# Performance work log

Hardware: AMD Instinct MI355X
Metric: run time of the kernel (lower is better)

## Reference

```python
import jax, jax.numpy as jnp
import numpy as np

H = 8        # num_heads
KNN = 16     # k nearest neighbors
D = 256      # input_dim
LN_EPS = 1e-5


def _make_params(key, D):
    ks = jax.random.split(key, 10)
    def lin(k, din, dout):
        k1, k2 = jax.random.split(k)
        lim = 1.0 / np.sqrt(din)
        W = jax.random.uniform(k1, (din, dout), jnp.float32, -lim, lim)
        b = jax.random.uniform(k2, (dout,), jnp.float32, -lim, lim)
        return W, b
    Wq, bq = lin(ks[0], D, D)
    Wk, bk = lin(ks[1], D, D)
    Wv, bv = lin(ks[2], D, D)
    Wo1, bo1 = lin(ks[3], D, D)
    ln_g = jnp.ones((D,), jnp.float32)
    ln_b = jnp.zeros((D,), jnp.float32)
    Wo2, bo2 = lin(ks[4], D, D)
    return dict(Wq=Wq, bq=bq, Wk=Wk, bk=bk, Wv=Wv, bv=bv,
                Wo1=Wo1, bo1=bo1, ln_g=ln_g, ln_b=ln_b, Wo2=Wo2, bo2=bo2)


def setup_inputs() -> dict:
    key = jax.random.key(0)
    k1, k2, k3, k4, k5 = jax.random.split(key, 5)
    B, N, M = 2, 2048, 4096
    inp = {
        "src": jax.random.normal(k1, (B, N, 3), jnp.float32),
        "tgt": jax.random.normal(k2, (B, M, 3), jnp.float32),
        "src_fea": jax.random.normal(k3, (B, N, D), jnp.float32),
        "tgt_fea": jax.random.normal(k4, (B, M, D), jnp.float32),
    }
    inp.update(_make_params(k5, D))
    return inp


def _cdist(x, y):
    # Euclidean distance [B,N,M], matching torch.cdist(p=2)
    x2 = jnp.sum(x * x, axis=-1, keepdims=True)          # [B,N,1]
    y2 = jnp.sum(y * y, axis=-1, keepdims=True)          # [B,M,1]
    sq = x2 + jnp.swapaxes(y2, -1, -2) - 2.0 * jnp.einsum('bnc,bmc->bnm', x, y)
    return jnp.sqrt(jnp.maximum(sq, 0.0))


def _layernorm(x, g, b):
    mu = jnp.mean(x, axis=-1, keepdims=True)
    var = jnp.mean((x - mu) ** 2, axis=-1, keepdims=True)
    return (x - mu) * jax.lax.rsqrt(var + LN_EPS) * g + b


def reference(src, tgt, src_fea, tgt_fea, Wq, bq, Wk, bk, Wv, bv,
              Wo1, bo1, ln_g, ln_b, Wo2, bo2):
    B, N, Dm = src_fea.shape
    M = tgt.shape[1]
    dk = Dm // H
    scale = dk ** (-0.5)

    # kNN mask: distances [B,N,M], topk smallest -> boolean mask
    dist = _cdist(src, tgt)
    _, knn_idx = jax.lax.top_k(-dist, KNN)               # [B,N,KNN]
    bi = jnp.arange(B)[:, None, None]
    ni = jnp.arange(N)[None, :, None]
    mask = jnp.zeros((B, N, M), bool).at[bi, ni, knn_idx].set(True)

    # projections -> [B,H,*,dk]
    Q = (src_fea @ Wq + bq).reshape(B, N, H, dk).transpose(0, 2, 1, 3)
    K = (tgt_fea @ Wk + bk).reshape(B, M, H, dk).transpose(0, 2, 1, 3)
    V = (tgt_fea @ Wv + bv).reshape(B, M, H, dk).transpose(0, 2, 1, 3)

    scores = jnp.einsum('bhnd,bhmd->bhnm', Q, K) * scale
    scores = jnp.where(mask[:, None], scores, -jnp.inf)
    attn = jax.nn.softmax(scores, axis=-1)               # [B,H,N,M]

    out = jnp.einsum('bhnm,bhmd->bhnd', attn, V)
    out = out.transpose(0, 2, 1, 3).reshape(B, N, Dm)

    x = out + src_fea
    h = jax.nn.relu(_layernorm(x @ Wo1 + bo1, ln_g, ln_b))
    updated = h @ Wo2 + bo2

    avg_attn = jnp.mean(attn, axis=1)                    # [B,N,M]
    return updated, avg_attn
```

## Files before the change

kernel.cpp:

```cpp
#include <hip/hip_runtime.h>
#include <math.h>

#define BB 2
#define NN 2048
#define MM 4096
#define DD 256
#define HH 8
#define DK 32
#define KNN 16

typedef __attribute__((ext_vector_type(8))) short short8;
typedef __attribute__((ext_vector_type(4))) short short4v;
typedef __attribute__((ext_vector_type(4))) float f32x4;
typedef unsigned long long u64;
typedef unsigned short u16;

static __device__ __forceinline__ u16 f2bf(float f) {
    union { float f; unsigned u; } v; v.f = f;
    unsigned r = v.u + 0x7FFF + ((v.u >> 16) & 1);
    return (u16)(r >> 16);
}
static __device__ __forceinline__ float bf2f(u16 u) {
    union { unsigned u; float f; } v; v.u = ((unsigned)u) << 16;
    return v.f;
}

__global__ __launch_bounds__(256)
void prep(const float* W0, const float* W1, const float* W2, const float* W3, const float* W4,
          u16* O0, u16* O1, u16* O2, u16* O3, u16* O4,
          const float* __restrict__ tgt, float4* __restrict__ tgt4)
{
    __shared__ float tile[64][65];
    const int bid = blockIdx.x;
    const int t = threadIdx.x;
    if (bid >= 80) {
        const int i = (bid - 80) * 256 + t;
        const float x = tgt[i * 3 + 0], y = tgt[i * 3 + 1], z = tgt[i * 3 + 2];
        float4 o; o.x = x; o.y = y; o.z = z; o.w = x * x + y * y + z * z;
        tgt4[i] = o;
        return;
    }
    const int m = bid >> 4, tl = bid & 15;
    const int tr = (tl >> 2) * 64, tc = (tl & 3) * 64;
    const float* W = m == 0 ? W0 : m == 1 ? W1 : m == 2 ? W2 : m == 3 ? W3 : W4;
    u16*        O = m == 0 ? O0 : m == 1 ? O1 : m == 2 ? O2 : m == 3 ? O3 : O4;
    const int c = t & 63, r4 = t >> 6;
    #pragma unroll
    for (int i = 0; i < 16; ++i) {
        const int r = (r4 << 4) + i;
        tile[r][c] = W[(size_t)(tr + r) * 256 + tc + c];
    }
    __syncthreads();
    #pragma unroll
    for (int i = 0; i < 16; ++i) {
        const int cc = (r4 << 4) + i;
        O[(size_t)(tc + cc) * 256 + tr + c] = f2bf(tile[c][cc]);
    }
}

static __device__ __forceinline__ void gemm64_body(
    const float* __restrict__ A, size_t row0, const u16* __restrict__ WT, int col0,
    u16* As, u16* Bs, int t, f32x4 acc[2][2])
{
    const int lane = t & 63, w = t >> 6;
    const int wr = (w >> 1) * 32, wc = (w & 1) * 32;
    for (int k0 = 0; k0 < 256; k0 += 64) {
        #pragma unroll
        for (int e = 0; e < 2; ++e) {
            const int flat = t + (e << 8);
            const int r = flat >> 3, kc = (flat & 7) << 3;
            const int off = ((r << 7) + (kc << 1)) ^ ((r & 7) << 4);
            const float* ap = A + (row0 + r) * 256 + k0 + kc;
            float4 a0 = *(const float4*)ap;
            float4 a1 = *(const float4*)(ap + 4);
            short8 s;
            s[0] = (short)f2bf(a0.x); s[1] = (short)f2bf(a0.y);
            s[2] = (short)f2bf(a0.z); s[3] = (short)f2bf(a0.w);
            s[4] = (short)f2bf(a1.x); s[5] = (short)f2bf(a1.y);
            s[6] = (short)f2bf(a1.z); s[7] = (short)f2bf(a1.w);
            *(short8*)((char*)As + off) = s;
            *(short8*)((char*)Bs + off) = *(const short8*)(WT + (size_t)(col0 + r) * 256 + k0 + kc);
        }
        __syncthreads();
        #pragma unroll
        for (int kk = 0; kk < 64; kk += 32) {
            const int kbo = (kk + ((lane >> 4) << 3)) << 1;
            short8 af[2], bfr[2];
            #pragma unroll
            for (int i = 0; i < 2; ++i) {
                const int ra = wr + (i << 4) + (lane & 15);
                af[i]  = *(const short8*)((const char*)As + (((ra << 7) + kbo) ^ ((ra & 7) << 4)));
                const int rb = wc + (i << 4) + (lane & 15);
                bfr[i] = *(const short8*)((const char*)Bs + (((rb << 7) + kbo) ^ ((rb & 7) << 4)));
            }
            #pragma unroll
            for (int mi = 0; mi < 2; ++mi)
                #pragma unroll
                for (int ni = 0; ni < 2; ++ni)
                    acc[mi][ni] = __builtin_amdgcn_mfma_f32_16x16x32_bf16(af[mi], bfr[ni], acc[mi][ni], 0, 0, 0);
        }
        __syncthreads();
    }
}

__global__ __launch_bounds__(256, 4)
void mega_kernel(const float* __restrict__ src, const float* __restrict__ tgt,
                 const float4* __restrict__ tgt4,
                 int* __restrict__ knn_idx,
                 const float* __restrict__ tgt_fea, const float* __restrict__ src_fea,
                 const u16* __restrict__ WTq, const u16* __restrict__ WTkv,
                 const float* __restrict__ bq, const float* __restrict__ bk,
                 const float* __restrict__ bv,
                 float* __restrict__ Qb, u16* __restrict__ Kbf, u16* __restrict__ Vbf,
                 float* __restrict__ avg)
{
    __shared__ u16 As[64 * 64];
    __shared__ u16 Bs[64 * 64];
    const int bid = blockIdx.x;
    const int t = threadIdx.x;
    const int lane = t & 63;
    const int lid = bid / 11;
    const int role = bid % 11;

    if (role < 4) {
        const int kb = lid * 4 + role;
        const int bn = (kb << 2) + (t >> 6);
        const int b = bn >> 11;
        const float* sp = src + (size_t)bn * 3;
        const float px = sp[0], py = sp[1], pz = sp[2];
        const float x2 = px * px + py * py + pz * pz;
        const float4* t4 = tgt4 + (size_t)b * MM;
        unsigned key[64];
        unsigned s0 = 0xFFFFFFFFu, s1 = 0xFFFFFFFFu;
        #pragma unroll
        for (int j = 0; j < 64; ++j) {
            const int m = (j << 6) + lane;
            const float4 tp = t4[m];
            const float dot = px * tp.x + py * tp.y + pz * tp.z;
            float d = (x2 + tp.w) - 2.0f * dot;
            d = d > 0.f ? d : 0.f;
            const unsigned k = ((unsigned)fminf(d * 32768.0f, 1048574.0f) << 12) | (unsigned)m;
            key[j] = k;
            const unsigned hi = k > s0 ? k : s0;
            s0 = k < s0 ? k : s0;
            s1 = hi < s1 ? hi : s1;
        }
        unsigned lastPop = 0, mykey = 0;
        for (int sel = 0; sel < 20; ++sel) {
            if (s0 == 0xFFFFFFFFu) {
                unsigned bst = 0xFFFFFFFFu;
                #pragma unroll
                for (int j = 0; j < 64; ++j) {
                    const unsigned k = key[j];
                    bst = (k > lastPop && k < bst) ? k : bst;
                }
                s0 = bst;
            }
            unsigned best = s0;
            #pragma unroll
            for (int s2 = 32; s2; s2 >>= 1) {
                const unsigned o = __shfl_xor(best, s2, 64);
                best = o < best ? o : best;
            }
            if (lane == sel) mykey = best;
            if (s0 == best) {
                lastPop = s0;
                s0 = s1;
                s1 = 0xFFFFFFFFu;
            }
        }
        const int midx = (int)(mykey & 0xFFFu);
        const float* tb = tgt + (size_t)b * MM * 3;
        u64 ex = ~0ULL;
        if (lane < 20) {
            const float* tp = tb + (size_t)midx * 3;
            const double pxd = px, pyd = py, pzd = pz;
            const double tx = tp[0], ty = tp[1], tz = tp[2];
            const double x2d = pxd * pxd + pyd * pyd + pzd * pzd;
            const double y2d = tx * tx + ty * ty + tz * tz;
            const double dtd = pxd * tx + pyd * ty + pzd * tz;
            double dd = (x2d + y2d) - 2.0 * dtd;
            dd = dd > 0.0 ? dd : 0.0;
            ex = (((u64)__double_as_longlong(dd)) & ~0xFFFULL) | (u64)midx;
        }
        int rank = 0;
        #pragma unroll
        for (int i = 0; i < 20; ++i) {
            const u64 o = __shfl(ex, i, 64);
            rank += (o < ex) ? 1 : 0;
        }
        if (lane < 20 && rank < 16)
            knn_idx[(size_t)bn * KNN + rank] = midx;
        return;
    }

    if (role < 8) {
        const int kvb = lid * 4 + (role - 4);
        const size_t row0 = (size_t)(kvb >> 3) * 64;
        const int col0 = (kvb & 7) * 64;
        f32x4 acc[2][2] = {};
        gemm64_body(tgt_fea, row0, WTkv, col0, As, Bs, t, acc);
        const int w = t >> 6;
        const int wr = (w >> 1) * 32, wc = (w & 1) * 32;
        const bool isv = col0 >= 256;
        u16* ob = isv ? Vbf : Kbf;
        const float* bs = isv ? bv : bk;
        const int cb = (isv ? col0 - 256 : col0) + wc;
        const int cq = lane & 15, rq = (lane >> 4) << 2;
        #pragma unroll
        for (int ni = 0; ni < 2; ++ni) {
            const int c = cb + (ni << 4) + cq;
            const float bval = bs[c];
            #pragma unroll
            for (int mi = 0; mi < 2; ++mi) {
                const size_t r = row0 + wr + (mi << 4) + rq;
                #pragma unroll
                for (int e = 0; e < 4; ++e)
                    ob[(r + e) * 256 + c] = f2bf(acc[mi][ni][e] + bval);
            }
        }
        return;
    }

    if (role == 8) {
        const int qb = lid;
        const size_t row0 = (size_t)(qb >> 2) * 64;
        const int col0 = (qb & 3) * 64;
        f32x4 acc[2][2] = {};
        gemm64_body(src_fea, row0, WTq, col0, As, Bs, t, acc);
        const int w = t >> 6;
        const int wr = (w >> 1) * 32, wc = (w & 1) * 32;
        const int cq = lane & 15, rq = (lane >> 4) << 2;
        #pragma unroll
        for (int ni = 0; ni < 2; ++ni) {
            const int c = col0 + wc + (ni << 4) + cq;
            const float bval = bq[c];
            #pragma unroll
            for (int mi = 0; mi < 2; ++mi) {
                const size_t rbase = (row0 + wr + (mi << 4) + rq) * 256 + c;
                #pragma unroll
                for (int e = 0; e < 4; ++e)
                    Qb[rbase + (size_t)e * 256] = acc[mi][ni][e] + bval;
            }
        }
        return;
    }

    {
        const int zb = lid * 2 + (role - 9);
        f32x4 z = {0.f, 0.f, 0.f, 0.f};
        f32x4* pz = (f32x4*)avg;
        const int base = zb * 256 + t;
        #pragma unroll
        for (int i = 0; i < 32; ++i)
            pz[base + i * 131072] = z;
    }
}

__global__ __launch_bounds__(256)
void tail_kernel(const float* __restrict__ Q, const u16* __restrict__ Kb,
                 const u16* __restrict__ Vb, const int* __restrict__ knn_idx,
                 const float* __restrict__ src_fea,
                 const u16* __restrict__ WTo1, const float* __restrict__ bo1,
                 const float* __restrict__ lng, const float* __restrict__ lnb,
                 const u16* __restrict__ WTo2, const float* __restrict__ bo2,
                 float* __restrict__ updated, float* __restrict__ avg_attn)
{
    __shared__ float q_sh[4][256];
    __shared__ float pw_sh[4][8][17];
    __shared__ int   idx_sh[4][16];
    __shared__ u16   Xs[16 * 256];
    __shared__ u16   Hs[16 * 256];
    __shared__ float2 red2[4][4];
    const int t = threadIdx.x;
    const int w = t >> 6, lane = t & 63;
    const int r0 = blockIdx.x << 2;
    const int bn = r0 + w;
    const int b = bn >> 11;
    const int h = lane >> 3, k2 = lane & 7;

    {
        unsigned* xz = (unsigned*)Xs;
        unsigned* hz = (unsigned*)Hs;
        #pragma unroll
        for (int i = 0; i < 6; ++i) {
            xz[512 + t + i * 256] = 0u;
            hz[512 + t + i * 256] = 0u;
        }
    }

    *(float4*)&q_sh[w][lane << 2] = *(const float4*)(Q + (size_t)bn * 256 + (lane << 2));
    const int ia = knn_idx[(size_t)bn * KNN + k2];
    const int ib = knn_idx[(size_t)bn * KNN + 8 + k2];

    const u16* Ka = Kb + ((size_t)b * MM + ia) * 256 + h * DK;
    const u16* Kc = Kb + ((size_t)b * MM + ib) * 256 + h * DK;
    const float* qh = &q_sh[w][h * DK];
    float s0 = 0.f, s1 = 0.f;
    #pragma unroll
    for (int j = 0; j < DK; j += 8) {
        const short8 ka = *(const short8*)(Ka + j);
        const short8 kc = *(const short8*)(Kc + j);
        #pragma unroll
        for (int e = 0; e < 8; ++e) {
            const float qv = qh[j + e];
            s0 = fmaf(qv, bf2f((u16)ka[e]), s0);
            s1 = fmaf(qv, bf2f((u16)kc[e]), s1);
        }
    }
    s0 *= 0.17677669529663688f;
    s1 *= 0.17677669529663688f;

    float mx = fmaxf(s0, s1);
    mx = fmaxf(mx, __shfl_xor(mx, 1, 64));
    mx = fmaxf(mx, __shfl_xor(mx, 2, 64));
    mx = fmaxf(mx, __shfl_xor(mx, 4, 64));
    const float e0 = expf(s0 - mx), e1 = expf(s1 - mx);
    float sum = e0 + e1;
    sum += __shfl_xor(sum, 1, 64);
    sum += __shfl_xor(sum, 2, 64);
    sum += __shfl_xor(sum, 4, 64);
    const float inv = 1.0f / sum;
    const float p0 = e0 * inv, p1 = e1 * inv;

    float a0 = p0, a1 = p1;
    a0 += __shfl_xor(a0, 8, 64);  a1 += __shfl_xor(a1, 8, 64);
    a0 += __shfl_xor(a0, 16, 64); a1 += __shfl_xor(a1, 16, 64);
    a0 += __shfl_xor(a0, 32, 64); a1 += __shfl_xor(a1, 32, 64);
    if (h == 0) {
        avg_attn[(size_t)bn * MM + ia] = a0 * 0.125f;
        avg_attn[(size_t)bn * MM + ib] = a1 * 0.125f;
        idx_sh[w][k2] = ia;
        idx_sh[w][8 + k2] = ib;
    }
    pw_sh[w][h][k2] = p0;
    pw_sh[w][h][8 + k2] = p1;

    {
        const int d0 = lane << 2;
        const int h2 = lane >> 3;
        float o0 = 0.f, o1 = 0.f, o2 = 0.f, o3 = 0.f;
        #pragma unroll
        for (int k = 0; k < KNN; ++k) {
            const float p = pw_sh[w][h2][k];
            const int ik = idx_sh[w][k];
            const short4v v4 = *(const short4v*)(Vb + ((size_t)b * MM + ik) * 256 + d0);
            o0 = fmaf(p, bf2f((u16)v4[0]), o0);
            o1 = fmaf(p, bf2f((u16)v4[1]), o1);
            o2 = fmaf(p, bf2f((u16)v4[2]), o2);
            o3 = fmaf(p, bf2f((u16)v4[3]), o3);
        }
        const float4 sf = *(const float4*)(src_fea + (size_t)bn * 256 + d0);
        short4v xo;
        xo[0] = (short)f2bf(o0 + sf.x);
        xo[1] = (short)f2bf(o1 + sf.y);
        xo[2] = (short)f2bf(o2 + sf.z);
        xo[3] = (short)f2bf(o3 + sf.w);
        const int off = ((w << 9) + (d0 << 1)) ^ ((w & 7) << 4);
        *(short4v*)((char*)Xs + off) = xo;
    }
    __syncthreads();

    const int cq = lane & 15, ks = lane >> 4;
    f32x4 acc1[4] = {};
    #pragma unroll
    for (int s = 0; s < 4; ++s) {
        const int colB = (w << 6) + (s << 4) + cq;
        const u16* bp = WTo1 + (size_t)colB * 256;
        #pragma unroll
        for (int kk = 0; kk < 256; kk += 32) {
            const int k8 = kk + (ks << 3);
            const short8 af = *(const short8*)((const char*)Xs + (((cq << 9) + (k8 << 1)) ^ ((cq & 7) << 4)));
            const short8 bfrg = *(const short8*)(bp + k8);
            acc1[s] = __builtin_amdgcn_mfma_f32_16x16x32_bf16(af, bfrg, acc1[s], 0, 0, 0);
        }
        const float bval = bo1[colB];
        #pragma unroll
        for (int e = 0; e < 4; ++e) acc1[s][e] += bval;
    }
    {
        #pragma unroll
        for (int e = 0; e < 4; ++e) {
            float v = acc1[0][e] + acc1[1][e] + acc1[2][e] + acc1[3][e];
            float vv = acc1[0][e]*acc1[0][e] + acc1[1][e]*acc1[1][e]
                     + acc1[2][e]*acc1[2][e] + acc1[3][e]*acc1[3][e];
            v += __shfl_xor(v, 1, 64); vv += __shfl_xor(vv, 1, 64);
            v += __shfl_xor(v, 2, 64); vv += __shfl_xor(vv, 2, 64);
            v += __shfl_xor(v, 4, 64); vv += __shfl_xor(vv, 4, 64);
            v += __shfl_xor(v, 8, 64); vv += __shfl_xor(vv, 8, 64);
            if (ks == 0 && cq == 0) {
                float2 pr; pr.x = v; pr.y = vv;
                red2[w][e] = pr;
            }
        }
    }
    __syncthreads();
    if (ks == 0) {
        float g4[4], b4[4];
        #pragma unroll
        for (int s = 0; s < 4; ++s) {
            const int colB = (w << 6) + (s << 4) + cq;
            g4[s] = lng[colB]; b4[s] = lnb[colB];
        }
        #pragma unroll
        for (int e = 0; e < 4; ++e) {
            float S1 = 0.f, S2 = 0.f;
            #pragma unroll
            for (int w2 = 0; w2 < 4; ++w2) {
                const float2 pr = red2[w2][e];
                S1 += pr.x; S2 += pr.y;
            }
            const float mean = S1 * (1.0f / 256.0f);
            const float var = S2 * (1.0f / 256.0f) - mean * mean;
            const float rstd = 1.0f / sqrtf(var + 1e-5f);
            #pragma unroll
            for (int s = 0; s < 4; ++s) {
                const int colB = (w << 6) + (s << 4) + cq;
                const float y = (acc1[s][e] - mean) * rstd * g4[s] + b4[s];
                const int off = ((e << 9) + (colB << 1)) ^ ((e & 7) << 4);
                *(u16*)((char*)Hs + off) = f2bf(fmaxf(y, 0.0f));
            }
        }
    }
    __syncthreads();

    #pragma unroll
    for (int s = 0; s < 4; ++s) {
        const int colB = (w << 6) + (s << 4) + cq;
        const u16* bp = WTo2 + (size_t)colB * 256;
        f32x4 acc2 = {};
        #pragma unroll
        for (int kk = 0; kk < 256; kk += 32) {
            const int k8 = kk + (ks << 3);
            const short8 af = *(const short8*)((const char*)Hs + (((cq << 9) + (k8 << 1)) ^ ((cq & 7) << 4)));
            const short8 bfrg = *(const short8*)(bp + k8);
            acc2 = __builtin_amdgcn_mfma_f32_16x16x32_bf16(af, bfrg, acc2, 0, 0, 0);
        }
        if (ks == 0) {
            const float bval = bo2[colB];
            #pragma unroll
            for (int e = 0; e < 4; ++e)
                updated[(size_t)(r0 + e) * 256 + colB] = acc2[e] + bval;
        }
    }
}

extern "C" void kernel_launch(void* const* d_in, const int* in_sizes, int n_in,
                              void* d_out, int out_size, void* d_ws, size_t ws_size,
                              hipStream_t stream) {
    const float* src     = (const float*)d_in[0];
    const float* tgt     = (const float*)d_in[1];
    const float* src_fea = (const float*)d_in[2];
    const float* tgt_fea = (const float*)d_in[3];
    const float* Wq  = (const float*)d_in[4];   const float* bq  = (const float*)d_in[5];
    const float* Wk  = (const float*)d_in[6];   const float* bk  = (const float*)d_in[7];
    const float* Wv  = (const float*)d_in[8];   const float* bv  = (const float*)d_in[9];
    const float* Wo1 = (const float*)d_in[10];  const float* bo1 = (const float*)d_in[11];
    const float* lng = (const float*)d_in[12];  const float* lnb = (const float*)d_in[13];
    const float* Wo2 = (const float*)d_in[14];  const float* bo2 = (const float*)d_in[15];
    (void)in_sizes; (void)n_in; (void)out_size; (void)ws_size;

    float* out     = (float*)d_out;
    float* updated = out;
    float* avg     = out + (size_t)BB * NN * DD;

    char* p = (char*)d_ws;
    u16* WTq  = (u16*)p;   p += 256 * 256 * 2;
    u16* WTk  = (u16*)p;   p += 256 * 256 * 2;
    u16* WTv  = (u16*)p;   p += 256 * 256 * 2;
    u16* WTo1 = (u16*)p;   p += 256 * 256 * 2;
    u16* WTo2 = (u16*)p;   p += 256 * 256 * 2;
    float* Qb = (float*)p; p += (size_t)BB * NN * DD * 4;
    u16* Kbf  = (u16*)p;   p += (size_t)BB * MM * DD * 2;
    u16* Vbf  = (u16*)p;   p += (size_t)BB * MM * DD * 2;
    int* knn  = (int*)p;   p += (size_t)BB * NN * KNN * 4;
    float4* tgt4 = (float4*)p; p += (size_t)BB * MM * 16;

    dim3 blk(256);
    prep<<<112, blk, 0, stream>>>(Wq, Wk, Wv, Wo1, Wo2, WTq, WTk, WTv, WTo1, WTo2,
                                  tgt, tgt4);
    mega_kernel<<<2816, blk, 0, stream>>>(src, tgt, tgt4, knn, tgt_fea, src_fea, WTq, WTk,
                                          bq, bk, bv, Qb, Kbf, Vbf, avg);
    tail_kernel<<<1024, blk, 0, stream>>>(Qb, Kbf, Vbf, knn, src_fea,
                                          WTo1, bo1, lng, lnb, WTo2, bo2,
                                          updated, avg);
}
```

Baseline: 184.4 us.

## Widen KV projection tiles to 64x128 and process 8 rows per tail block

In the mega kernel, the K/V projection blocks now compute 64x128 output tiles instead of 64x64. This halves the number of KV blocks and reuses each converted tgt_fea A-tile across twice as many columns, cutting redundant fp32 loads and bf16 conversions. The tail kernel moves to 512 threads handling 8 query rows per block, so each Wo1/Wo2 weight fragment read is shared across more rows. The LayerNorm reduction is reworked for 8 warps. In exchange it uses more registers and shared memory per block, and there are fewer blocks, which may lower occupancy.

```diff
diff --git a/kernel.cpp b/kernel.cpp
--- a/kernel.cpp
+++ b/kernel.cpp
@@ -58,51 +58,6 @@
     }
 }
 
-static __device__ __forceinline__ void gemm64_body(
-    const float* __restrict__ A, size_t row0, const u16* __restrict__ WT, int col0,
-    u16* As, u16* Bs, int t, f32x4 acc[2][2])
-{
-    const int lane = t & 63, w = t >> 6;
-    const int wr = (w >> 1) * 32, wc = (w & 1) * 32;
-    for (int k0 = 0; k0 < 256; k0 += 64) {
-        #pragma unroll
-        for (int e = 0; e < 2; ++e) {
-            const int flat = t + (e << 8);
-            const int r = flat >> 3, kc = (flat & 7) << 3;
-            const int off = ((r << 7) + (kc << 1)) ^ ((r & 7) << 4);
-            const float* ap = A + (row0 + r) * 256 + k0 + kc;
-            float4 a0 = *(const float4*)ap;
-            float4 a1 = *(const float4*)(ap + 4);
-            short8 s;
-            s[0] = (short)f2bf(a0.x); s[1] = (short)f2bf(a0.y);
-            s[2] = (short)f2bf(a0.z); s[3] = (short)f2bf(a0.w);
-            s[4] = (short)f2bf(a1.x); s[5] = (short)f2bf(a1.y);
-            s[6] = (short)f2bf(a1.z); s[7] = (short)f2bf(a1.w);
-            *(short8*)((char*)As + off) = s;
-            *(short8*)((char*)Bs + off) = *(const short8*)(WT + (size_t)(col0 + r) * 256 + k0 + kc);
-        }
-        __syncthreads();
-        #pragma unroll
-        for (int kk = 0; kk < 64; kk += 32) {
-            const int kbo = (kk + ((lane >> 4) << 3)) << 1;
-            short8 af[2], bfr[2];
-            #pragma unroll
-            for (int i = 0; i < 2; ++i) {
-                const int ra = wr + (i << 4) + (lane & 15);
-                af[i]  = *(const short8*)((const char*)As + (((ra << 7) + kbo) ^ ((ra & 7) << 4)));
-                const int rb = wc + (i << 4) + (lane & 15);
-                bfr[i] = *(const short8*)((const char*)Bs + (((rb << 7) + kbo) ^ ((rb & 7) << 4)));
-            }
-            #pragma unroll
-            for (int mi = 0; mi < 2; ++mi)
-                #pragma unroll
-                for (int ni = 0; ni < 2; ++ni)
-                    acc[mi][ni] = __builtin_amdgcn_mfma_f32_16x16x32_bf16(af[mi], bfr[ni], acc[mi][ni], 0, 0, 0);
-        }
-        __syncthreads();
-    }
-}
-
 __global__ __launch_bounds__(256, 4)
 void mega_kernel(const float* __restrict__ src, const float* __restrict__ tgt,
                  const float4* __restrict__ tgt4,
@@ -115,12 +70,12 @@
                  float* __restrict__ avg)
 {
     __shared__ u16 As[64 * 64];
-    __shared__ u16 Bs[64 * 64];
+    __shared__ u16 Bs[128 * 64];
     const int bid = blockIdx.x;
     const int t = threadIdx.x;
     const int lane = t & 63;
-    const int lid = bid / 11;
-    const int role = bid % 11;
+    const int lid = bid / 9;
+    const int role = bid % 9;
 
     if (role < 4) {
         const int kb = lid * 4 + role;
@@ -194,21 +149,66 @@
         return;
     }
 
-    if (role < 8) {
-        const int kvb = lid * 4 + (role - 4);
-        const size_t row0 = (size_t)(kvb >> 3) * 64;
-        const int col0 = (kvb & 7) * 64;
-        f32x4 acc[2][2] = {};
-        gemm64_body(tgt_fea, row0, WTkv, col0, As, Bs, t, acc);
+    if (role < 6) {
+        const int kvb = lid * 2 + (role - 4);
+        const size_t row0 = (size_t)(kvb >> 2) * 64;
+        const int col0 = (kvb & 3) * 128;
         const int w = t >> 6;
-        const int wr = (w >> 1) * 32, wc = (w & 1) * 32;
+        const int wr = (w >> 1) * 32, wc = (w & 1) * 64;
+        f32x4 acc[2][4] = {};
+        for (int k0 = 0; k0 < 256; k0 += 64) {
+            #pragma unroll
+            for (int e = 0; e < 2; ++e) {
+                const int flat = t + (e << 8);
+                const int r = flat >> 3, kc = (flat & 7) << 3;
+                const int off = ((r << 7) + (kc << 1)) ^ ((r & 7) << 4);
+                const float* ap = tgt_fea + (row0 + r) * 256 + k0 + kc;
+                float4 a0 = *(const float4*)ap;
+                float4 a1 = *(const float4*)(ap + 4);
+                short8 s;
+                s[0] = (short)f2bf(a0.x); s[1] = (short)f2bf(a0.y);
+                s[2] = (short)f2bf(a0.z); s[3] = (short)f2bf(a0.w);
+                s[4] = (short)f2bf(a1.x); s[5] = (short)f2bf(a1.y);
+                s[6] = (short)f2bf(a1.z); s[7] = (short)f2bf(a1.w);
+                *(short8*)((char*)As + off) = s;
+            }
+            #pragma unroll
+            for (int e = 0; e < 4; ++e) {
+                const int flat = t + (e << 8);
+                const int r = flat >> 3, kc = (flat & 7) << 3;
+                const int off = ((r << 7) + (kc << 1)) ^ ((r & 7) << 4);
+                *(short8*)((char*)Bs + off) = *(const short8*)(WTkv + (size_t)(col0 + r) * 256 + k0 + kc);
+            }
+            __syncthreads();
+            #pragma unroll
+            for (int kk = 0; kk < 64; kk += 32) {
+                const int kbo = (kk + ((lane >> 4) << 3)) << 1;
+                short8 af[2], bfr[4];
+                #pragma unroll
+                for (int i = 0; i < 2; ++i) {
+                    const int ra = wr + (i << 4) + (lane & 15);
+                    af[i] = *(const short8*)((const char*)As + (((ra << 7) + kbo) ^ ((ra & 7) << 4)));
+                }
+                #pragma unroll
+                for (int i = 0; i < 4; ++i) {
+                    const int rb = wc + (i << 4) + (lane & 15);
+                    bfr[i] = *(const short8*)((const char*)Bs + (((rb << 7) + kbo) ^ ((rb & 7) << 4)));
+                }
+                #pragma unroll
+                for (int mi = 0; mi < 2; ++mi)
+                    #pragma unroll
+                    for (int ni = 0; ni < 4; ++ni)
+                        acc[mi][ni] = __builtin_amdgcn_mfma_f32_16x16x32_bf16(af[mi], bfr[ni], acc[mi][ni], 0, 0, 0);
+            }
+            __syncthreads();
+        }
         const bool isv = col0 >= 256;
         u16* ob = isv ? Vbf : Kbf;
         const float* bs = isv ? bv : bk;
         const int cb = (isv ? col0 - 256 : col0) + wc;
         const int cq = lane & 15, rq = (lane >> 4) << 2;
         #pragma unroll
-        for (int ni = 0; ni < 2; ++ni) {
+        for (int ni = 0; ni < 4; ++ni) {
             const int c = cb + (ni << 4) + cq;
             const float bval = bs[c];
             #pragma unroll
@@ -222,14 +222,50 @@
         return;
     }
 
-    if (role == 8) {
+    if (role == 6) {
         const int qb = lid;
         const size_t row0 = (size_t)(qb >> 2) * 64;
         const int col0 = (qb & 3) * 64;
-        f32x4 acc[2][2] = {};
-        gemm64_body(src_fea, row0, WTq, col0, As, Bs, t, acc);
         const int w = t >> 6;
         const int wr = (w >> 1) * 32, wc = (w & 1) * 32;
+        f32x4 acc[2][2] = {};
+        for (int k0 = 0; k0 < 256; k0 += 64) {
+            #pragma unroll
+            for (int e = 0; e < 2; ++e) {
+                const int flat = t + (e << 8);
+                const int r = flat >> 3, kc = (flat & 7) << 3;
+                const int off = ((r << 7) + (kc << 1)) ^ ((r & 7) << 4);
+                const float* ap = src_fea + (row0 + r) * 256 + k0 + kc;
+                float4 a0 = *(const float4*)ap;
+                float4 a1 = *(const float4*)(ap + 4);
+                short8 s;
+                s[0] = (short)f2bf(a0.x); s[1] = (short)f2bf(a0.y);
+                s[2] = (short)f2bf(a0.z); s[3] = (short)f2bf(a0.w);
+                s[4] = (short)f2bf(a1.x); s[5] = (short)f2bf(a1.y);
+                s[6] = (short)f2bf(a1.z); s[7] = (short)f2bf(a1.w);
+                *(short8*)((char*)As + off) = s;
+                *(short8*)((char*)Bs + off) = *(const short8*)(WTq + (size_t)(col0 + r) * 256 + k0 + kc);
+            }
+            __syncthreads();
+            #pragma unroll
+            for (int kk = 0; kk < 64; kk += 32) {
+                const int kbo = (kk + ((lane >> 4) << 3)) << 1;
+                short8 af[2], bfr[2];
+                #pragma unroll
+                for (int i = 0; i < 2; ++i) {
+                    const int ra = wr + (i << 4) + (lane & 15);
+                    af[i]  = *(const short8*)((const char*)As + (((ra << 7) + kbo) ^ ((ra & 7) << 4)));
+                    const int rb = wc + (i << 4) + (lane & 15);
+                    bfr[i] = *(const short8*)((const char*)Bs + (((rb << 7) + kbo) ^ ((rb & 7) << 4)));
+                }
+                #pragma unroll
+                for (int mi = 0; mi < 2; ++mi)
+                    #pragma unroll
+                    for (int ni = 0; ni < 2; ++ni)
+                        acc[mi][ni] = __builtin_amdgcn_mfma_f32_16x16x32_bf16(af[mi], bfr[ni], acc[mi][ni], 0, 0, 0);
+            }
+            __syncthreads();
+        }
         const int cq = lane & 15, rq = (lane >> 4) << 2;
         #pragma unroll
         for (int ni = 0; ni < 2; ++ni) {
@@ -247,7 +283,7 @@
     }
 
     {
-        const int zb = lid * 2 + (role - 9);
+        const int zb = lid * 2 + (role - 7);
         f32x4 z = {0.f, 0.f, 0.f, 0.f};
         f32x4* pz = (f32x4*)avg;
         const int base = zb * 256 + t;
@@ -257,7 +293,7 @@
     }
 }
 
-__global__ __launch_bounds__(256)
+__global__ __launch_bounds__(512)
 void tail_kernel(const float* __restrict__ Q, const u16* __restrict__ Kb,
                  const u16* __restrict__ Vb, const int* __restrict__ knn_idx,
                  const float* __restrict__ src_fea,
@@ -266,15 +302,15 @@
                  const u16* __restrict__ WTo2, const float* __restrict__ bo2,
                  float* __restrict__ updated, float* __restrict__ avg_attn)
 {
-    __shared__ float q_sh[4][256];
-    __shared__ float pw_sh[4][8][17];
-    __shared__ int   idx_sh[4][16];
+    __shared__ float q_sh[8][256];
+    __shared__ float pw_sh[8][8][17];
+    __shared__ int   idx_sh[8][16];
     __shared__ u16   Xs[16 * 256];
     __shared__ u16   Hs[16 * 256];
-    __shared__ float2 red2[4][4];
+    __shared__ float2 red2[8][8];
     const int t = threadIdx.x;
     const int w = t >> 6, lane = t & 63;
-    const int r0 = blockIdx.x << 2;
+    const int r0 = blockIdx.x << 3;
     const int bn = r0 + w;
     const int b = bn >> 11;
     const int h = lane >> 3, k2 = lane & 7;
@@ -283,9 +319,9 @@
         unsigned* xz = (unsigned*)Xs;
         unsigned* hz = (unsigned*)Hs;
         #pragma unroll
-        for (int i = 0; i < 6; ++i) {
-            xz[512 + t + i * 256] = 0u;
-            hz[512 + t + i * 256] = 0u;
+        for (int i = 0; i < 2; ++i) {
+            xz[1024 + t + i * 512] = 0u;
+            hz[1024 + t + i * 512] = 0u;
         }
     }
 
@@ -362,10 +398,10 @@
     __syncthreads();
 
     const int cq = lane & 15, ks = lane >> 4;
-    f32x4 acc1[4] = {};
+    f32x4 acc1[2] = {};
     #pragma unroll
-    for (int s = 0; s < 4; ++s) {
-        const int colB = (w << 6) + (s << 4) + cq;
+    for (int s = 0; s < 2; ++s) {
+        const int colB = (w << 5) + (s << 4) + cq;
         const u16* bp = WTo1 + (size_t)colB * 256;
         #pragma unroll
         for (int kk = 0; kk < 256; kk += 32) {
@@ -381,43 +417,43 @@
     {
         #pragma unroll
         for (int e = 0; e < 4; ++e) {
-            float v = acc1[0][e] + acc1[1][e] + acc1[2][e] + acc1[3][e];
-            float vv = acc1[0][e]*acc1[0][e] + acc1[1][e]*acc1[1][e]
-                     + acc1[2][e]*acc1[2][e] + acc1[3][e]*acc1[3][e];
+            float v  = acc1[0][e] + acc1[1][e];
+            float vv = acc1[0][e]*acc1[0][e] + acc1[1][e]*acc1[1][e];
             v += __shfl_xor(v, 1, 64); vv += __shfl_xor(vv, 1, 64);
             v += __shfl_xor(v, 2, 64); vv += __shfl_xor(vv, 2, 64);
             v += __shfl_xor(v, 4, 64); vv += __shfl_xor(vv, 4, 64);
             v += __shfl_xor(v, 8, 64); vv += __shfl_xor(vv, 8, 64);
-            if (ks == 0 && cq == 0) {
+            if (cq == 0 && ks < 2) {
                 float2 pr; pr.x = v; pr.y = vv;
-                red2[w][e] = pr;
+                red2[w][(ks << 2) + e] = pr;
             }
         }
     }
     __syncthreads();
-    if (ks == 0) {
-        float g4[4], b4[4];
-        #pragma unroll
-        for (int s = 0; s < 4; ++s) {
-            const int colB = (w << 6) + (s << 4) + cq;
-            g4[s] = lng[colB]; b4[s] = lnb[colB];
+    if (ks < 2) {
+        float g2[2], b2[2];
+        #pragma unroll
+        for (int s = 0; s < 2; ++s) {
+            const int colB = (w << 5) + (s << 4) + cq;
+            g2[s] = lng[colB]; b2[s] = lnb[colB];
         }
         #pragma unroll
         for (int e = 0; e < 4; ++e) {
+            const int r = (ks << 2) + e;
             float S1 = 0.f, S2 = 0.f;
             #pragma unroll
-            for (int w2 = 0; w2 < 4; ++w2) {
-                const float2 pr = red2[w2][e];
+            for (int w2 = 0; w2 < 8; ++w2) {
+                const float2 pr = red2[w2][r];
                 S1 += pr.x; S2 += pr.y;
             }
             const float mean = S1 * (1.0f / 256.0f);
             const float var = S2 * (1.0f / 256.0f) - mean * mean;
             const float rstd = 1.0f / sqrtf(var + 1e-5f);
             #pragma unroll
-            for (int s = 0; s < 4; ++s) {
-                const int colB = (w << 6) + (s << 4) + cq;
-                const float y = (acc1[s][e] - mean) * rstd * g4[s] + b4[s];
-                const int off = ((e << 9) + (colB << 1)) ^ ((e & 7) << 4);
+            for (int s = 0; s < 2; ++s) {
+                const int colB = (w << 5) + (s << 4) + cq;
+                const float y = (acc1[s][e] - mean) * rstd * g2[s] + b2[s];
+                const int off = ((r << 9) + (colB << 1)) ^ ((r & 7) << 4);
                 *(u16*)((char*)Hs + off) = f2bf(fmaxf(y, 0.0f));
             }
         }
@@ -425,8 +461,8 @@
     __syncthreads();
 
     #pragma unroll
-    for (int s = 0; s < 4; ++s) {
-        const int colB = (w << 6) + (s << 4) + cq;
+    for (int s = 0; s < 2; ++s) {
+        const int colB = (w << 5) + (s << 4) + cq;
         const u16* bp = WTo2 + (size_t)colB * 256;
         f32x4 acc2 = {};
         #pragma unroll
@@ -436,11 +472,11 @@
             const short8 bfrg = *(const short8*)(bp + k8);
             acc2 = __builtin_amdgcn_mfma_f32_16x16x32_bf16(af, bfrg, acc2, 0, 0, 0);
         }
-        if (ks == 0) {
+        if (ks < 2) {
             const float bval = bo2[colB];
             #pragma unroll
             for (int e = 0; e < 4; ++e)
-                updated[(size_t)(r0 + e) * 256 + colB] = acc2[e] + bval;
+                updated[(size_t)(r0 + (ks << 2) + e) * 256 + colB] = acc2[e] + bval;
         }
     }
 }
@@ -479,9 +515,9 @@
     dim3 blk(256);
     prep<<<112, blk, 0, stream>>>(Wq, Wk, Wv, Wo1, Wo2, WTq, WTk, WTv, WTo1, WTo2,
                                   tgt, tgt4);
-    mega_kernel<<<2816, blk, 0, stream>>>(src, tgt, tgt4, knn, tgt_fea, src_fea, WTq, WTk,
+    mega_kernel<<<2304, blk, 0, stream>>>(src, tgt, tgt4, knn, tgt_fea, src_fea, WTq, WTk,
                                           bq, bk, bv, Qb, Kbf, Vbf, avg);
-    tail_kernel<<<1024, blk, 0, stream>>>(Qb, Kbf, Vbf, knn, src_fea,
-                                          WTo1, bo1, lng, lnb, WTo2, bo2,
-                                          updated, avg);
+    tail_kernel<<<512, dim3(512), 0, stream>>>(Qb, Kbf, Vbf, knn, src_fea,
+                                               WTo1, bo1, lng, lnb, WTo2, bo2,
+                                               updated, avg);
 }
```

Result: faster. 167.5 us (-9.2%).
